# Performance work log

Measured on AMD Instinct MI355X. Metric: run time of the kernel, lower is better.

The kernel has to match this reference:

```python
import jax, jax.numpy as jnp
import numpy as np

B, T, D, H = 2, 2048, 1024, 16

def setup_inputs() -> dict:
    key = jax.random.key(0)
    k0, k1, k2, k3 = jax.random.split(key, 4)
    s = 0.02
    return {
        "x": jax.random.normal(k0, (B, T, D), dtype=jnp.float32),
        "Wqkv": jax.random.normal(k1, (3 * D, D), dtype=jnp.float32) * s,
        "Wout": jax.random.normal(k2, (D, D), dtype=jnp.float32) * s,
        "bout": jax.random.normal(k3, (D,), dtype=jnp.float32) * s,
    }

def reference(x, Wqkv, Wout, bout):
    b, t, d = x.shape
    h = H
    dh = d // h
    qkv = x @ Wqkv.T  # [b,t,3d]
    q, k, v = jnp.split(qkv, 3, axis=-1)
    def merge_heads(z):
        return z.reshape(b, t, h, dh).transpose(0, 2, 1, 3)  # [b,h,t,dh]
    q, k, v = map(merge_heads, (q, k, v))
    scale = dh ** -0.5
    dots = jnp.einsum('bhid,bhjd->bhij', q, k) * scale  # [b,h,t,t]
    causal_mask = jnp.triu(jnp.ones((t, t), dtype=bool), 1)
    dots = jnp.where(causal_mask, -jnp.inf, dots)
    attn = jax.nn.softmax(dots, axis=-1)
    out = jnp.einsum('bhij,bhjd->bhid', attn, v)  # [b,h,t,dh]
    out = out.transpose(0, 2, 1, 3).reshape(b, t, d)
    return out @ Wout.T + bout
```

## Files before the change

### kernel.cpp

```cpp
#include <hip/hip_runtime.h>
#include <hip/hip_bf16.h>
#include <math.h>

typedef __bf16 bf16x8 __attribute__((ext_vector_type(8)));
typedef float f32x4 __attribute__((ext_vector_type(4)));
typedef unsigned short u16;
typedef unsigned int u32;

#define EXP2F(x) __builtin_amdgcn_exp2f(x)

constexpr int Bz = 2, T = 2048, D = 1024, H = 16;
constexpr int M = Bz * T;
constexpr int NQKV = 3 * D;
constexpr float SCALE2 = 0.125f * 1.44269504089f;

#define GLD_LDS16(g, l) __builtin_amdgcn_global_load_lds( \
    (__attribute__((address_space(1))) void*)(g),          \
    (__attribute__((address_space(3))) void*)(l), 16, 0, 0)

__global__ void cvt_all_kernel(const float* __restrict__ x,
                               const float* __restrict__ wq,
                               const float* __restrict__ wo,
                               u16* __restrict__ xb, u16* __restrict__ wqb,
                               u16* __restrict__ wob) {
  constexpr int NX = M * D / 4;
  constexpr int NQ = NQKV * D / 4;
  constexpr int NW = D * D / 4;
  constexpr int TOT = NX + NQ + NW;
  int i = blockIdx.x * blockDim.x + threadIdx.x;
  int stride = gridDim.x * blockDim.x;
  for (; i < TOT; i += stride) {
    const float4* src;
    u16* dst;
    int j;
    if (i < NX) { src = (const float4*)x; dst = xb; j = i; }
    else if (i < NX + NQ) { src = (const float4*)wq; dst = wqb; j = i - NX; }
    else { src = (const float4*)wo; dst = wob; j = i - NX - NQ; }
    float4 f = src[j];
    ushort4 u;
    u.x = __builtin_bit_cast(u16, (__bf16)f.x);
    u.y = __builtin_bit_cast(u16, (__bf16)f.y);
    u.z = __builtin_bit_cast(u16, (__bf16)f.z);
    u.w = __builtin_bit_cast(u16, (__bf16)f.w);
    ((ushort4*)dst)[j] = u;
  }
}

template <bool FP32OUT, bool QSCALE>
__global__ __launch_bounds__(256, 2)
void gemm_bt(const u16* __restrict__ A, const u16* __restrict__ Bm,
             u16* __restrict__ outb, float* __restrict__ outf,
             const float* __restrict__ bias, int K, int ldc) {
  __shared__ __align__(16) u16 sA[128 * 64];
  __shared__ __align__(16) u16 sB[128 * 64];
  const int tid = threadIdx.x;
  const int lane = tid & 63;
  const int wid = tid >> 6;
  const int wr = wid >> 1, wc = wid & 1;

  const int nwg = gridDim.x * gridDim.y;
  const int flat = blockIdx.y * gridDim.x + blockIdx.x;
  const int cpx = nwg >> 3;
  const int swz = (flat & 7) * cpx + (flat >> 3);
  const int bx = swz % gridDim.x;
  const int by = swz / gridDim.x;

  const int row0 = by * 128;
  const int col0 = bx * 128;

  f32x4 acc[4][4];
#pragma unroll
  for (int m = 0; m < 4; ++m)
#pragma unroll
    for (int n = 0; n < 4; ++n) acc[m][n] = (f32x4){0.f, 0.f, 0.f, 0.f};

  const int nk = K >> 6;
  for (int kt = 0; kt < nk; ++kt) {
    const int k0 = kt << 6;
#pragma unroll
    for (int i = 0; i < 4; ++i) {
      int off = i * 4096 + tid * 16;
      int r = off >> 7;
      int cs = (off >> 4) & 7;
      int c = cs ^ (r & 7);
      const u16* ga = A + (size_t)(row0 + r) * K + k0 + c * 8;
      const u16* gb = Bm + (size_t)(col0 + r) * K + k0 + c * 8;
      u16* la = sA + (i * 4096 + (tid & ~63) * 16) / 2;
      u16* lb = sB + (i * 4096 + (tid & ~63) * 16) / 2;
      GLD_LDS16(ga, la);
      GLD_LDS16(gb, lb);
    }
    __syncthreads();
#pragma unroll
    for (int kk = 0; kk < 2; ++kk) {
      bf16x8 af[4], bfv[4];
#pragma unroll
      for (int m = 0; m < 4; ++m) {
        int r = wr * 64 + m * 16 + (lane & 15);
        int cs = (kk * 4 + (lane >> 4)) ^ (r & 7);
        af[m] = *(const bf16x8*)(sA + r * 64 + cs * 8);
      }
#pragma unroll
      for (int n = 0; n < 4; ++n) {
        int r = wc * 64 + n * 16 + (lane & 15);
        int cs = (kk * 4 + (lane >> 4)) ^ (r & 7);
        bfv[n] = *(const bf16x8*)(sB + r * 64 + cs * 8);
      }
#pragma unroll
      for (int m = 0; m < 4; ++m)
#pragma unroll
        for (int n = 0; n < 4; ++n)
          acc[m][n] = __builtin_amdgcn_mfma_f32_16x16x32_bf16(
              af[m], bfv[n], acc[m][n], 0, 0, 0);
    }
    __syncthreads();
  }

  const int orow0 = row0 + wr * 64;
  const int ocol0 = col0 + wc * 64;
#pragma unroll
  for (int m = 0; m < 4; ++m)
#pragma unroll
    for (int n = 0; n < 4; ++n)
#pragma unroll
      for (int j = 0; j < 4; ++j) {
        int rr = orow0 + m * 16 + (lane >> 4) * 4 + j;
        int cc = ocol0 + n * 16 + (lane & 15);
        if (FP32OUT) {
          outf[(size_t)rr * ldc + cc] = acc[m][n][j] + bias[cc];
        } else {
          float v = acc[m][n][j];
          if (QSCALE && cc < D) v *= SCALE2;
          outb[(size_t)rr * ldc + cc] = __builtin_bit_cast(u16, (__bf16)v);
        }
      }
}

__global__ __launch_bounds__(256, 3)
void flash_kernel(const u16* __restrict__ qkv, u16* __restrict__ attn_out) {
  __shared__ __align__(16) u16 sK[2][64 * 64];
  __shared__ __align__(16) u16 sVt[2][64 * 72];
  __shared__ __align__(16) u16 sP[4][16][72];

  const int tid = threadIdx.x;
  const int lane = tid & 63;
  const int l15 = lane & 15;
  const int hi = lane >> 4;
  const int w = tid >> 6;
  const int bh = blockIdx.x;
  const int b = bh >> 4, h = bh & 15;
  const int qt = (gridDim.y - 1) - blockIdx.y;
  const int q0 = qt * 64;
  const int nv = qt + 1;

  const size_t base = (size_t)b * T * 3072;
  const u16* qp = qkv + base + 0 * 1024 + h * 64;
  const u16* kp = qkv + base + 1 * 1024 + h * 64;
  const u16* vp = qkv + base + 2 * 1024 + h * 64;

  ushort4 vr[2][2];
  auto stageK = [&](u16* dst, int kt) {
#pragma unroll
    for (int i = 0; i < 2; ++i) {
      int off = i * 4096 + tid * 16;
      int r = off >> 7;
      int cs = (off >> 4) & 7;
      int c = cs ^ (r & 7);
      GLD_LDS16(kp + (size_t)(kt * 64 + r) * 3072 + c * 8,
                dst + (i * 4096 + (tid & ~63) * 16) / 2);
    }
  };
  auto loadV = [&](int kt) {
#pragma unroll
    for (int i = 0; i < 2; ++i) {
      const u16* gsrc = vp + (size_t)(kt * 64 + lane) * 3072 + (i * 4 + w) * 8;
      vr[i][0] = ((const ushort4*)gsrc)[0];
      vr[i][1] = ((const ushort4*)gsrc)[1];
    }
  };
  auto writeV = [&](u16* dst) {
#pragma unroll
    for (int i = 0; i < 2; ++i) {
      int c = i * 4 + w;
      dst[(c * 8 + 0) * 72 + lane] = vr[i][0].x;
      dst[(c * 8 + 1) * 72 + lane] = vr[i][0].y;
      dst[(c * 8 + 2) * 72 + lane] = vr[i][0].z;
      dst[(c * 8 + 3) * 72 + lane] = vr[i][0].w;
      dst[(c * 8 + 4) * 72 + lane] = vr[i][1].x;
      dst[(c * 8 + 5) * 72 + lane] = vr[i][1].y;
      dst[(c * 8 + 6) * 72 + lane] = vr[i][1].z;
      dst[(c * 8 + 7) * 72 + lane] = vr[i][1].w;
    }
  };

  bf16x8 qf[2];
#pragma unroll
  for (int kk = 0; kk < 2; ++kk)
    qf[kk] = *(const bf16x8*)(qp + (size_t)(q0 + w * 16 + l15) * 3072 +
                              kk * 32 + hi * 8);

  f32x4 o_acc[4];
#pragma unroll
  for (int n = 0; n < 4; ++n) o_acc[n] = (f32x4){0.f, 0.f, 0.f, 0.f};
  float m2 = -INFINITY, l_run = 0.f;

  stageK(sK[0], 0);
  loadV(0);
  writeV(sVt[0]);
  __syncthreads();

  for (int v = 0; v < nv; ++v) {
    const int cur = v & 1;
    const int k0 = v * 64;
    if (v + 1 < nv) {
      stageK(sK[cur ^ 1], v + 1);
      loadV(v + 1);
    }

    bf16x8 kf[2][4];
#pragma unroll
    for (int kk = 0; kk < 2; ++kk)
#pragma unroll
      for (int n = 0; n < 4; ++n) {
        int rk = n * 16 + l15;
        int cs = (kk * 4 + hi) ^ (rk & 7);
        kf[kk][n] = *(const bf16x8*)(&sK[cur][rk * 64 + cs * 8]);
      }
    bf16x8 vf[2][4];
#pragma unroll
    for (int ks = 0; ks < 2; ++ks)
#pragma unroll
      for (int n = 0; n < 4; ++n)
        vf[ks][n] = *(const bf16x8*)(
            &sVt[cur][(n * 16 + l15) * 72 + ks * 32 + hi * 8]);

    f32x4 sc[4];
#pragma unroll
    for (int n = 0; n < 4; ++n) sc[n] = (f32x4){0.f, 0.f, 0.f, 0.f};
    __builtin_amdgcn_s_setprio(1);
#pragma unroll
    for (int kk = 0; kk < 2; ++kk)
#pragma unroll
      for (int n = 0; n < 4; ++n)
        sc[n] = __builtin_amdgcn_mfma_f32_16x16x32_bf16(kf[kk][n], qf[kk],
                                                        sc[n], 0, 0, 0);
    __builtin_amdgcn_s_setprio(0);

    const bool diag = (v == nv - 1);
    const int qrow = q0 + w * 16 + l15;
    float mx = -INFINITY;
#pragma unroll
    for (int n = 0; n < 4; ++n)
#pragma unroll
      for (int r = 0; r < 4; ++r) {
        float sv = sc[n][r];
        if (diag) {
          int kpos = k0 + n * 16 + hi * 4 + r;
          if (kpos > qrow) sv = -INFINITY;
        }
        sc[n][r] = sv;
        mx = fmaxf(mx, sv);
      }
    mx = fmaxf(mx, __shfl_xor(mx, 16, 64));
    mx = fmaxf(mx, __shfl_xor(mx, 32, 64));

    const bool skip = __all(mx <= m2);
    float alpha = 1.f;
    if (!skip) {
      float mn = fmaxf(m2, mx);
      alpha = EXP2F(m2 - mn);
      m2 = mn;
    }

    float sum = 0.f;
#pragma unroll
    for (int n = 0; n < 4; ++n) {
      float p0 = EXP2F(sc[n][0] - m2);
      float p1 = EXP2F(sc[n][1] - m2);
      float p2 = EXP2F(sc[n][2] - m2);
      float p3 = EXP2F(sc[n][3] - m2);
      sum += (p0 + p1) + (p2 + p3);
      u32 w01 = ((u32)__builtin_bit_cast(u16, (__bf16)p1) << 16) |
                __builtin_bit_cast(u16, (__bf16)p0);
      u32 w23 = ((u32)__builtin_bit_cast(u16, (__bf16)p3) << 16) |
                __builtin_bit_cast(u16, (__bf16)p2);
      *(u32*)(&sP[w][l15][n * 16 + hi * 4 + 0]) = w01;
      *(u32*)(&sP[w][l15][n * 16 + hi * 4 + 2]) = w23;
    }
    l_run = l_run * alpha + sum;

    if (!skip) {
      float ab[4];
#pragma unroll
      for (int j = 0; j < 4; ++j) ab[j] = __shfl(alpha, hi * 4 + j, 64);
#pragma unroll
      for (int n = 0; n < 4; ++n)
#pragma unroll
        for (int j = 0; j < 4; ++j) o_acc[n][j] *= ab[j];
    }
    __builtin_amdgcn_s_setprio(1);
#pragma unroll
    for (int ks = 0; ks < 2; ++ks) {
      bf16x8 pf = *(const bf16x8*)(&sP[w][l15][ks * 32 + hi * 8]);
#pragma unroll
      for (int n = 0; n < 4; ++n)
        o_acc[n] = __builtin_amdgcn_mfma_f32_16x16x32_bf16(pf, vf[ks][n],
                                                           o_acc[n], 0, 0, 0);
    }
    __builtin_amdgcn_s_setprio(0);

    if (v + 1 < nv) writeV(sVt[cur ^ 1]);
    if (v + 1 < nv) __syncthreads();
  }

  l_run += __shfl_xor(l_run, 16, 64);
  l_run += __shfl_xor(l_run, 32, 64);

#pragma unroll
  for (int j = 0; j < 4; ++j) {
    float lj = __shfl(l_run, hi * 4 + j, 64);
    float inv = 1.f / lj;
    int row = q0 + w * 16 + hi * 4 + j;
#pragma unroll
    for (int n = 0; n < 4; ++n) {
      int cc = h * 64 + n * 16 + l15;
      attn_out[((size_t)b * T + row) * 1024 + cc] =
          __builtin_bit_cast(u16, (__bf16)(o_acc[n][j] * inv));
    }
  }
}

extern "C" void kernel_launch(void* const* d_in, const int* in_sizes, int n_in,
                              void* d_out, int out_size, void* d_ws,
                              size_t ws_size, hipStream_t stream) {
  (void)in_sizes; (void)n_in; (void)out_size; (void)ws_size;
  const float* x = (const float*)d_in[0];
  const float* Wqkv = (const float*)d_in[1];
  const float* Wout = (const float*)d_in[2];
  const float* bout = (const float*)d_in[3];
  float* out = (float*)d_out;

  char* ws = (char*)d_ws;
  u16* x_bf = (u16*)(ws + 0);
  u16* wqkv_bf = (u16*)(ws + 8388608);
  u16* wout_bf = (u16*)(ws + 14680064);
  u16* qkvb = (u16*)(ws + 16777216);
  u16* aout = (u16*)(ws + 41943040);

  cvt_all_kernel<<<2048, 256, 0, stream>>>(x, Wqkv, Wout, x_bf, wqkv_bf,
                                           wout_bf);

  gemm_bt<false, true><<<dim3(NQKV / 128, M / 128), 256, 0, stream>>>(
      x_bf, wqkv_bf, qkvb, nullptr, nullptr, D, NQKV);

  flash_kernel<<<dim3(Bz * H, T / 64), 256, 0, stream>>>(qkvb, aout);

  gemm_bt<true, false><<<dim3(D / 128, M / 128), 256, 0, stream>>>(
      aout, wout_bf, nullptr, out, bout, D, D);
}
```

Before: 107.5 us.

## Process two 64-row query groups per flash block to reuse staged K/V tiles

Each flash-attention block now handles 128 query rows as two 64-row groups that share every staged K and V tile in LDS. Each wave keeps two sets of online-softmax state and accumulators. The first group is skipped on the final key tile, which lies past its diagonal. This halves the grid and the K/V global loads per query row. In exchange it raises register pressure, which could lower occupancy under the launch bound, and leaves fewer blocks to balance the causal workload.

```diff
diff --git a/kernel.cpp b/kernel.cpp
--- a/kernel.cpp
+++ b/kernel.cpp
@@ -140,7 +140,7 @@
 void flash_kernel(const u16* __restrict__ qkv, u16* __restrict__ attn_out) {
   __shared__ __align__(16) u16 sK[2][64 * 64];
   __shared__ __align__(16) u16 sVt[2][64 * 72];
-  __shared__ __align__(16) u16 sP[4][16][72];
+  __shared__ __align__(16) u16 sP[4][2][16][72];
 
   const int tid = threadIdx.x;
   const int lane = tid & 63;
@@ -150,8 +150,8 @@
   const int bh = blockIdx.x;
   const int b = bh >> 4, h = bh & 15;
   const int qt = (gridDim.y - 1) - blockIdx.y;
-  const int q0 = qt * 64;
-  const int nv = qt + 1;
+  const int q0 = qt * 128;
+  const int nv = 2 * qt + 2;
 
   const size_t base = (size_t)b * T * 3072;
   const u16* qp = qkv + base + 0 * 1024 + h * 64;
@@ -193,16 +193,22 @@
     }
   };
 
-  bf16x8 qf[2];
-#pragma unroll
-  for (int kk = 0; kk < 2; ++kk)
-    qf[kk] = *(const bf16x8*)(qp + (size_t)(q0 + w * 16 + l15) * 3072 +
-                              kk * 32 + hi * 8);
-
-  f32x4 o_acc[4];
-#pragma unroll
-  for (int n = 0; n < 4; ++n) o_acc[n] = (f32x4){0.f, 0.f, 0.f, 0.f};
-  float m2 = -INFINITY, l_run = 0.f;
+  bf16x8 qf[2][2];
+#pragma unroll
+  for (int g = 0; g < 2; ++g)
+#pragma unroll
+    for (int kk = 0; kk < 2; ++kk)
+      qf[g][kk] = *(const bf16x8*)(qp +
+          (size_t)(q0 + g * 64 + w * 16 + l15) * 3072 + kk * 32 + hi * 8);
+
+  f32x4 o_acc[2][4];
+#pragma unroll
+  for (int g = 0; g < 2; ++g)
+#pragma unroll
+    for (int n = 0; n < 4; ++n) o_acc[g][n] = (f32x4){0.f, 0.f, 0.f, 0.f};
+  float m2[2] = {-INFINITY, -INFINITY};
+  float l_run[2] = {0.f, 0.f};
+  const int wl = w * 16 + l15;
 
   stageK(sK[0], 0);
   loadV(0);
@@ -211,11 +217,11 @@
 
   for (int v = 0; v < nv; ++v) {
     const int cur = v & 1;
-    const int k0 = v * 64;
     if (v + 1 < nv) {
       stageK(sK[cur ^ 1], v + 1);
       loadV(v + 1);
     }
+    const bool g0act = (v != nv - 1);
 
     bf16x8 kf[2][4];
 #pragma unroll
@@ -226,6 +232,75 @@
         int cs = (kk * 4 + hi) ^ (rk & 7);
         kf[kk][n] = *(const bf16x8*)(&sK[cur][rk * 64 + cs * 8]);
       }
+
+    f32x4 sc[2][4];
+#pragma unroll
+    for (int g = 0; g < 2; ++g)
+#pragma unroll
+      for (int n = 0; n < 4; ++n) sc[g][n] = (f32x4){0.f, 0.f, 0.f, 0.f};
+    __builtin_amdgcn_s_setprio(1);
+    if (g0act) {
+#pragma unroll
+      for (int kk = 0; kk < 2; ++kk)
+#pragma unroll
+        for (int n = 0; n < 4; ++n)
+          sc[0][n] = __builtin_amdgcn_mfma_f32_16x16x32_bf16(
+              kf[kk][n], qf[0][kk], sc[0][n], 0, 0, 0);
+    }
+#pragma unroll
+    for (int kk = 0; kk < 2; ++kk)
+#pragma unroll
+      for (int n = 0; n < 4; ++n)
+        sc[1][n] = __builtin_amdgcn_mfma_f32_16x16x32_bf16(
+            kf[kk][n], qf[1][kk], sc[1][n], 0, 0, 0);
+    __builtin_amdgcn_s_setprio(0);
+
+    float alpha[2];
+    bool skipg[2];
+#pragma unroll
+    for (int g = 0; g < 2; ++g) {
+      if (g == 0 && !g0act) { alpha[0] = 1.f; skipg[0] = true; continue; }
+      const bool diag = (v == 2 * qt + g);
+      float mx = -INFINITY;
+#pragma unroll
+      for (int n = 0; n < 4; ++n)
+#pragma unroll
+        for (int r = 0; r < 4; ++r) {
+          float sv = sc[g][n][r];
+          if (diag && (n * 16 + hi * 4 + r > wl)) sv = -INFINITY;
+          sc[g][n][r] = sv;
+          mx = fmaxf(mx, sv);
+        }
+      mx = fmaxf(mx, __shfl_xor(mx, 16, 64));
+      mx = fmaxf(mx, __shfl_xor(mx, 32, 64));
+
+      const bool skip = __all(mx <= m2[g]);
+      float al = 1.f;
+      if (!skip) {
+        float mn = fmaxf(m2[g], mx);
+        al = EXP2F(m2[g] - mn);
+        m2[g] = mn;
+      }
+      float sum = 0.f;
+#pragma unroll
+      for (int n = 0; n < 4; ++n) {
+        float p0 = EXP2F(sc[g][n][0] - m2[g]);
+        float p1 = EXP2F(sc[g][n][1] - m2[g]);
+        float p2 = EXP2F(sc[g][n][2] - m2[g]);
+        float p3 = EXP2F(sc[g][n][3] - m2[g]);
+        sum += (p0 + p1) + (p2 + p3);
+        u32 w01 = ((u32)__builtin_bit_cast(u16, (__bf16)p1) << 16) |
+                  __builtin_bit_cast(u16, (__bf16)p0);
+        u32 w23 = ((u32)__builtin_bit_cast(u16, (__bf16)p3) << 16) |
+                  __builtin_bit_cast(u16, (__bf16)p2);
+        *(u32*)(&sP[w][g][l15][n * 16 + hi * 4 + 0]) = w01;
+        *(u32*)(&sP[w][g][l15][n * 16 + hi * 4 + 2]) = w23;
+      }
+      l_run[g] = l_run[g] * al + sum;
+      alpha[g] = al;
+      skipg[g] = skip;
+    }
+
     bf16x8 vf[2][4];
 #pragma unroll
     for (int ks = 0; ks < 2; ++ks)
@@ -234,98 +309,50 @@
         vf[ks][n] = *(const bf16x8*)(
             &sVt[cur][(n * 16 + l15) * 72 + ks * 32 + hi * 8]);
 
-    f32x4 sc[4];
-#pragma unroll
-    for (int n = 0; n < 4; ++n) sc[n] = (f32x4){0.f, 0.f, 0.f, 0.f};
-    __builtin_amdgcn_s_setprio(1);
-#pragma unroll
-    for (int kk = 0; kk < 2; ++kk)
-#pragma unroll
-      for (int n = 0; n < 4; ++n)
-        sc[n] = __builtin_amdgcn_mfma_f32_16x16x32_bf16(kf[kk][n], qf[kk],
-                                                        sc[n], 0, 0, 0);
-    __builtin_amdgcn_s_setprio(0);
-
-    const bool diag = (v == nv - 1);
-    const int qrow = q0 + w * 16 + l15;
-    float mx = -INFINITY;
-#pragma unroll
-    for (int n = 0; n < 4; ++n)
-#pragma unroll
-      for (int r = 0; r < 4; ++r) {
-        float sv = sc[n][r];
-        if (diag) {
-          int kpos = k0 + n * 16 + hi * 4 + r;
-          if (kpos > qrow) sv = -INFINITY;
-        }
-        sc[n][r] = sv;
-        mx = fmaxf(mx, sv);
-      }
-    mx = fmaxf(mx, __shfl_xor(mx, 16, 64));
-    mx = fmaxf(mx, __shfl_xor(mx, 32, 64));
-
-    const bool skip = __all(mx <= m2);
-    float alpha = 1.f;
-    if (!skip) {
-      float mn = fmaxf(m2, mx);
-      alpha = EXP2F(m2 - mn);
-      m2 = mn;
-    }
-
-    float sum = 0.f;
-#pragma unroll
-    for (int n = 0; n < 4; ++n) {
-      float p0 = EXP2F(sc[n][0] - m2);
-      float p1 = EXP2F(sc[n][1] - m2);
-      float p2 = EXP2F(sc[n][2] - m2);
-      float p3 = EXP2F(sc[n][3] - m2);
-      sum += (p0 + p1) + (p2 + p3);
-      u32 w01 = ((u32)__builtin_bit_cast(u16, (__bf16)p1) << 16) |
-                __builtin_bit_cast(u16, (__bf16)p0);
-      u32 w23 = ((u32)__builtin_bit_cast(u16, (__bf16)p3) << 16) |
-                __builtin_bit_cast(u16, (__bf16)p2);
-      *(u32*)(&sP[w][l15][n * 16 + hi * 4 + 0]) = w01;
-      *(u32*)(&sP[w][l15][n * 16 + hi * 4 + 2]) = w23;
-    }
-    l_run = l_run * alpha + sum;
-
-    if (!skip) {
-      float ab[4];
-#pragma unroll
-      for (int j = 0; j < 4; ++j) ab[j] = __shfl(alpha, hi * 4 + j, 64);
-#pragma unroll
-      for (int n = 0; n < 4; ++n)
-#pragma unroll
-        for (int j = 0; j < 4; ++j) o_acc[n][j] *= ab[j];
-    }
-    __builtin_amdgcn_s_setprio(1);
-#pragma unroll
-    for (int ks = 0; ks < 2; ++ks) {
-      bf16x8 pf = *(const bf16x8*)(&sP[w][l15][ks * 32 + hi * 8]);
-#pragma unroll
-      for (int n = 0; n < 4; ++n)
-        o_acc[n] = __builtin_amdgcn_mfma_f32_16x16x32_bf16(pf, vf[ks][n],
-                                                           o_acc[n], 0, 0, 0);
-    }
-    __builtin_amdgcn_s_setprio(0);
+#pragma unroll
+    for (int g = 0; g < 2; ++g) {
+      if (g == 0 && !g0act) continue;
+      if (!skipg[g]) {
+        float ab[4];
+#pragma unroll
+        for (int j = 0; j < 4; ++j) ab[j] = __shfl(alpha[g], hi * 4 + j, 64);
+#pragma unroll
+        for (int n = 0; n < 4; ++n)
+#pragma unroll
+          for (int j = 0; j < 4; ++j) o_acc[g][n][j] *= ab[j];
+      }
+      __builtin_amdgcn_s_setprio(1);
+#pragma unroll
+      for (int ks = 0; ks < 2; ++ks) {
+        bf16x8 pf = *(const bf16x8*)(&sP[w][g][l15][ks * 32 + hi * 8]);
+#pragma unroll
+        for (int n = 0; n < 4; ++n)
+          o_acc[g][n] = __builtin_amdgcn_mfma_f32_16x16x32_bf16(
+              pf, vf[ks][n], o_acc[g][n], 0, 0, 0);
+      }
+      __builtin_amdgcn_s_setprio(0);
+    }
 
     if (v + 1 < nv) writeV(sVt[cur ^ 1]);
     if (v + 1 < nv) __syncthreads();
   }
 
-  l_run += __shfl_xor(l_run, 16, 64);
-  l_run += __shfl_xor(l_run, 32, 64);
-
-#pragma unroll
-  for (int j = 0; j < 4; ++j) {
-    float lj = __shfl(l_run, hi * 4 + j, 64);
-    float inv = 1.f / lj;
-    int row = q0 + w * 16 + hi * 4 + j;
-#pragma unroll
-    for (int n = 0; n < 4; ++n) {
-      int cc = h * 64 + n * 16 + l15;
-      attn_out[((size_t)b * T + row) * 1024 + cc] =
-          __builtin_bit_cast(u16, (__bf16)(o_acc[n][j] * inv));
+#pragma unroll
+  for (int g = 0; g < 2; ++g) {
+    float lr = l_run[g];
+    lr += __shfl_xor(lr, 16, 64);
+    lr += __shfl_xor(lr, 32, 64);
+#pragma unroll
+    for (int j = 0; j < 4; ++j) {
+      float lj = __shfl(lr, hi * 4 + j, 64);
+      float inv = 1.f / lj;
+      int row = q0 + g * 64 + w * 16 + hi * 4 + j;
+#pragma unroll
+      for (int n = 0; n < 4; ++n) {
+        int cc = h * 64 + n * 16 + l15;
+        attn_out[((size_t)b * T + row) * 1024 + cc] =
+            __builtin_bit_cast(u16, (__bf16)(o_acc[g][n][j] * inv));
+      }
     }
   }
 }
@@ -353,7 +380,7 @@
   gemm_bt<false, true><<<dim3(NQKV / 128, M / 128), 256, 0, stream>>>(
       x_bf, wqkv_bf, qkvb, nullptr, nullptr, D, NQKV);
 
-  flash_kernel<<<dim3(Bz * H, T / 64), 256, 0, stream>>>(qkvb, aout);
+  flash_kernel<<<dim3(Bz * H, T / 128), 256, 0, stream>>>(qkvb, aout);
 
   gemm_bt<true, false><<<dim3(D / 128, M / 128), 256, 0, stream>>>(
       aout, wout_bf, nullptr, out, bout, D, D);
```

Measured after the change: 122.0 us. 1.13x slower.
